# Kernel tuning notes

Hardware: AMD Instinct MI355X
Metric: run time of the kernel (lower is better)

The kernel has to match this reference:

```python
import jax, jax.numpy as jnp
import numpy as np

B, L, N = 4, 4096, 4096
COARSE_W, FINE_W = 1.0, 1000.0
PX_THRESH = 10.0


def setup_inputs() -> dict:
    key = jax.random.key(0)
    k1, k2, k3, k4, k5, k6 = jax.random.split(key, 6)
    # confidence matrix in (0,1] so log is finite
    cm_matrix = jax.random.uniform(k1, (B, L, L), jnp.float32, 1e-4, 1.0)
    # ground-truth match matrix: identity permutation (each i matches j=i)
    gt_matrix = jnp.tile(jnp.eye(L, dtype=jnp.float32)[None], (B, 1, 1))
    samples0 = jax.random.uniform(k2, (B, L, 2), jnp.float32, 0.0, 1000.0)
    samples1 = jax.random.uniform(k3, (B, L, 2), jnp.float32, 0.0, 1000.0)
    b_idx = jax.random.randint(k4, (N,), 0, B)
    i_idx = jax.random.randint(k5, (N,), 0, L)
    # predicted mkpts0 copied exactly from gt coords -> exact float equality match
    mkpts0 = jnp.concatenate([b_idx[:, None].astype(jnp.float32),
                              samples0[b_idx, i_idx]], axis=1)  # [N,3] = (b,x,y)
    noise = jax.random.normal(k6, (N, 2), jnp.float32) * 6.0  # some pass <10px gate, some not
    mkpts1 = samples1[b_idx, i_idx] + noise  # [N,2]
    return {"cm_matrix": cm_matrix, "gt_matrix": gt_matrix,
            "samples0": samples0, "samples1": samples1,
            "mkpts0": mkpts0, "mkpts1": mkpts1}


def _losses(cm_matrix, gt_matrix, samples0, samples1, mkpts0, mkpts1):
    b, l0, l1 = gt_matrix.shape
    # --- coarse CE loss ---
    coarse = (-gt_matrix * jnp.log(cm_matrix + 1e-6)).sum() / b

    # --- fine loss (vectorized first-match semantics) ---
    gt_mask = gt_matrix > 0                       # [B,L0,L1]
    gt_mask_v = gt_mask.any(axis=2)               # [B,L0] valid gt rows
    j_ids = jnp.argmax(gt_mask, axis=2)           # [B,L0] first True along j
    bb = jnp.broadcast_to(jnp.arange(b, dtype=samples0.dtype)[:, None], (b, l0))
    gt0 = jnp.concatenate([bb[..., None], samples0], axis=-1).reshape(b * l0, 3)  # (b,x,y)
    gt1 = jnp.take_along_axis(samples1, j_ids[:, :, None], axis=1).reshape(b * l0, 2)
    valid = gt_mask_v.reshape(-1)                 # [M]

    # eq[n,m]: predicted mkpts0[n] exactly equals gt row m (and row is valid)
    eq = (mkpts0[:, None, :] == gt0[None, :, :]).all(-1) & valid[None, :]  # [N,M]
    found = eq.any(axis=1)                        # [N]
    first = jnp.argmax(eq, axis=1)                # first matching gt row
    matched_gt1 = gt1[first]                      # [N,2]
    per_norm = jnp.linalg.norm(matched_gt1 - mkpts1, axis=1)  # [N]
    sel = found & (per_norm < PX_THRESH)
    cnt = sel.sum()
    fine = jnp.where(cnt > 0,
                     jnp.sum(per_norm * sel) / jnp.maximum(cnt, 1).astype(per_norm.dtype),
                     jnp.asarray(10.0, per_norm.dtype))
    fine = jnp.where(valid.any(), fine, jnp.asarray(1e-6, per_norm.dtype))
    # original does torch.tensor(loss, requires_grad=True): detaches from inputs
    fine = jax.lax.stop_gradient(fine)

    losses = COARSE_W * coarse + FINE_W * fine
    return jnp.stack([losses, coarse, fine])


def reference(cm_matrix, gt_matrix, samples0, samples1, mkpts0, mkpts1):
    # returns [losses, coarse_loss, fine_loss]
    return _losses(cm_matrix, gt_matrix, samples0, samples1, mkpts0, mkpts1)
```

## Files before the change

kernel.cpp:

```cpp
#include <hip/hip_runtime.h>
#include <climits>
#include <cstdint>


typedef float    f32x4 __attribute__((ext_vector_type(4)));
typedef unsigned u32x4 __attribute__((ext_vector_type(4)));

static constexpr int CGRID = 2048;
static constexpr int DEPTH = 8;

template <int LSHIFT>
__device__ __forceinline__ void coarse_proc4(
    float& local, const float* __restrict__ cm, int* __restrict__ jv,
    const f32x4 g, const unsigned v)
{
    const u32x4 u = __builtin_bit_cast(u32x4, g);
    if ((u.x | u.y | u.z | u.w) != 0u) {
        constexpr unsigned LMASK = (1u << LSHIFT) - 1u;
        const unsigned e   = v << 2;
        const unsigned row = e >> LSHIFT;
        const unsigned col = e & LMASK;
        #pragma unroll
        for (int k = 0; k < 4; ++k) {
            const float gk = g[k];
            if (gk != 0.0f) {
                local += gk * logf(__builtin_nontemporal_load(&cm[e + k]) + 1e-6f);
                if (gk > 0.0f) atomicMin(&jv[row], (int)(col + (unsigned)k));
            }
        }
    }
}

__device__ __forceinline__ void coarse_proc4_gen(
    float& local, const float* __restrict__ cm, int* __restrict__ jv,
    const f32x4 g, const unsigned v, const unsigned L)
{
    const u32x4 u = __builtin_bit_cast(u32x4, g);
    if ((u.x | u.y | u.z | u.w) != 0u) {
        const unsigned e   = v << 2;
        const unsigned row = e / L;
        const unsigned col = e - row * L;
        #pragma unroll
        for (int k = 0; k < 4; ++k) {
            const float gk = g[k];
            if (gk != 0.0f) {
                local += gk * logf(__builtin_nontemporal_load(&cm[e + k]) + 1e-6f);
                if (gk > 0.0f) atomicMin(&jv[row], (int)(col + (unsigned)k));
            }
        }
    }
}

template <int LSHIFT>
__global__ __launch_bounds__(256) void mc_coarse_flat(
    const float* __restrict__ cm, const float* __restrict__ gt,
    unsigned nvec, int* __restrict__ jv, float* __restrict__ partial)
{
    const unsigned stride = gridDim.x * blockDim.x;
    unsigned v = blockIdx.x * blockDim.x + threadIdx.x;
    const f32x4* __restrict__ g4 = reinterpret_cast<const f32x4*>(gt);

    float local = 0.0f;

    for (; v + (DEPTH - 1u) * stride < nvec; v += (unsigned)DEPTH * stride) {
        f32x4 g[DEPTH];
        #pragma unroll
        for (int m = 0; m < DEPTH; ++m)
            g[m] = __builtin_nontemporal_load(&g4[v + (unsigned)m * stride]);
        #pragma unroll
        for (int m = 0; m < DEPTH; ++m)
            coarse_proc4<LSHIFT>(local, cm, jv, g[m], v + (unsigned)m * stride);
    }
    for (; v < nvec; v += stride) {
        const f32x4 g = __builtin_nontemporal_load(&g4[v]);
        coarse_proc4<LSHIFT>(local, cm, jv, g, v);
    }

    #pragma unroll
    for (int o = 32; o; o >>= 1) local += __shfl_down(local, o);
    __shared__ float sc[4];
    if ((threadIdx.x & 63) == 0) sc[threadIdx.x >> 6] = local;
    __syncthreads();
    if (threadIdx.x == 0) partial[blockIdx.x] = sc[0] + sc[1] + sc[2] + sc[3];
}

__global__ __launch_bounds__(256) void mc_coarse_flat_gen(
    const float* __restrict__ cm, const float* __restrict__ gt,
    unsigned nvec, unsigned L, int* __restrict__ jv, float* __restrict__ partial)
{
    const unsigned stride = gridDim.x * blockDim.x;
    unsigned v = blockIdx.x * blockDim.x + threadIdx.x;
    const f32x4* __restrict__ g4 = reinterpret_cast<const f32x4*>(gt);

    float local = 0.0f;
    for (; v + (DEPTH - 1u) * stride < nvec; v += (unsigned)DEPTH * stride) {
        f32x4 g[DEPTH];
        #pragma unroll
        for (int m = 0; m < DEPTH; ++m)
            g[m] = __builtin_nontemporal_load(&g4[v + (unsigned)m * stride]);
        #pragma unroll
        for (int m = 0; m < DEPTH; ++m)
            coarse_proc4_gen(local, cm, jv, g[m], v + (unsigned)m * stride, L);
    }
    for (; v < nvec; v += stride) {
        const f32x4 g = __builtin_nontemporal_load(&g4[v]);
        coarse_proc4_gen(local, cm, jv, g, v, L);
    }

    #pragma unroll
    for (int o = 32; o; o >>= 1) local += __shfl_down(local, o);
    __shared__ float sc[4];
    if ((threadIdx.x & 63) == 0) sc[threadIdx.x >> 6] = local;
    __syncthreads();
    if (threadIdx.x == 0) partial[blockIdx.x] = sc[0] + sc[1] + sc[2] + sc[3];
}

__global__ __launch_bounds__(256) void mc_fine_kernel(
    const float* __restrict__ s0, const float* __restrict__ s1,
    const float* __restrict__ mk0, const float* __restrict__ mk1,
    const int* __restrict__ jv, int B, int L,
    float* __restrict__ pnbuf)
{
    const int n = blockIdx.x;
    const float bf = mk0[3 * n + 0];
    const float x  = mk0[3 * n + 1];
    const float y  = mk0[3 * n + 2];
    const int b = (int)bf;

    int best = INT_MAX;
    if ((float)b == bf && b >= 0 && b < B) {
        const float2* __restrict__ srow = reinterpret_cast<const float2*>(s0 + (size_t)b * L * 2);
        const int*    __restrict__ jrow = jv + (size_t)b * L;
        #pragma unroll 4
        for (int i = threadIdx.x; i < L; i += 256) {
            const float2 s = srow[i];
            if (s.x == x && s.y == y && jrow[i] < L) best = min(best, i);
        }
    }
    #pragma unroll
    for (int o = 32; o; o >>= 1) best = min(best, __shfl_down(best, o));

    __shared__ int sb[4];
    if ((threadIdx.x & 63) == 0) sb[threadIdx.x >> 6] = best;
    __syncthreads();

    if (threadIdx.x == 0) {
        best = min(min(sb[0], sb[1]), min(sb[2], sb[3]));
        float res = -1.0f;
        if (best != INT_MAX) {
            const int j = jv[(size_t)b * L + best];
            const float gx = s1[((size_t)b * L + j) * 2 + 0];
            const float gy = s1[((size_t)b * L + j) * 2 + 1];
            const float dx = gx - mk1[2 * n + 0];
            const float dy = gy - mk1[2 * n + 1];
            const float pn = sqrtf(dx * dx + dy * dy);
            if (pn < 10.0f) res = pn;
        }
        pnbuf[n] = res;
    }
}

__global__ __launch_bounds__(1024) void mc_finalize_kernel(
    const float* __restrict__ partial, int P,
    const int* __restrict__ jv, int M,
    const float* __restrict__ pnbuf, int N,
    float binv, int L, float* __restrict__ out)
{
    float csum = 0.0f, fsum = 0.0f;
    int vcnt = 0, fcnt = 0;
    for (int i = threadIdx.x; i < P; i += 1024) csum += partial[i];
    for (int i = threadIdx.x; i < M; i += 1024) vcnt += (jv[i] < L) ? 1 : 0;
    for (int i = threadIdx.x; i < N; i += 1024) {
        const float p = pnbuf[i];
        if (p >= 0.0f) { fsum += p; ++fcnt; }
    }
    #pragma unroll
    for (int o = 32; o; o >>= 1) {
        csum += __shfl_down(csum, o);
        vcnt += __shfl_down(vcnt, o);
        fsum += __shfl_down(fsum, o);
        fcnt += __shfl_down(fcnt, o);
    }
    __shared__ float sc[16], sf[16];
    __shared__ int   sv[16], sn[16];
    const int wid = threadIdx.x >> 6, lane = threadIdx.x & 63;
    if (lane == 0) { sc[wid] = csum; sv[wid] = vcnt; sf[wid] = fsum; sn[wid] = fcnt; }
    __syncthreads();
    if (threadIdx.x == 0) {
        float C = 0.0f, F = 0.0f; int V = 0, K = 0;
        const int nw = blockDim.x >> 6;
        for (int w = 0; w < nw; ++w) { C += sc[w]; V += sv[w]; F += sf[w]; K += sn[w]; }
        const float coarse = -C * binv;
        const float fine = (V > 0) ? ((K > 0) ? F / (float)K : 10.0f) : 1e-6f;
        out[0] = coarse + 1000.0f * fine;
        out[1] = coarse;
        out[2] = fine;
    }
}

extern "C" void kernel_launch(void* const* d_in, const int* in_sizes, int n_in,
                              void* d_out, int out_size, void* d_ws, size_t ws_size,
                              hipStream_t stream) {
    const float* cm  = (const float*)d_in[0];
    const float* gt  = (const float*)d_in[1];
    const float* s0  = (const float*)d_in[2];
    const float* s1  = (const float*)d_in[3];
    const float* mk0 = (const float*)d_in[4];
    const float* mk1 = (const float*)d_in[5];
    float* out = (float*)d_out;

    const int L = 2 * (in_sizes[0] / in_sizes[2]);
    const int B = in_sizes[2] / (2 * L);
    const int N = in_sizes[4] / 3;
    const int M = B * L;
    const unsigned nvec = (unsigned)(in_sizes[0] >> 2);

    int*   jv      = (int*)d_ws;
    float* pnbuf   = (float*)((char*)d_ws + (size_t)M * 4);
    float* partial = (float*)((char*)d_ws + (size_t)M * 4 + (size_t)N * 4);

    hipMemsetAsync(jv, 0x7F, (size_t)M * 4, stream);

    if (L == 4096) {
        mc_coarse_flat<12><<<CGRID, 256, 0, stream>>>(cm, gt, nvec, jv, partial);
    } else {
        mc_coarse_flat_gen<<<CGRID, 256, 0, stream>>>(cm, gt, nvec, (unsigned)L, jv, partial);
    }
    mc_fine_kernel<<<N, 256, 0, stream>>>(s0, s1, mk0, mk1, jv, B, L, pnbuf);
    mc_finalize_kernel<<<1, 1024, 0, stream>>>(partial, CGRID, jv, M, pnbuf, N,
                                               1.0f / (float)B, L, out);
}
```

Measured before the change: 468.9 us.

## Split coarse pass into sparse nonzero compaction scan and hit-processing kernel

The coarse pass becomes two kernels. The first streams the gt matrix and appends each nonzero (index, value) into a compacted list through a global atomic counter. The second kernel evaluates the log and atomicMin only for those entries, so the scan loop no longer carries log or cm-load work inline. The scan also switches from nontemporal loads to plain loads. Costs are a global atomic per nonzero, an extra launch and memset, and a spill path with float atomicAdd when the list capacity runs out.

Result: slower. 585.3 us (+24.8%).

```diff
diff --git a/kernel.cpp b/kernel.cpp
--- a/kernel.cpp
+++ b/kernel.cpp
@@ -6,107 +6,97 @@
 typedef float    f32x4 __attribute__((ext_vector_type(4)));
 typedef unsigned u32x4 __attribute__((ext_vector_type(4)));
 
-static constexpr int CGRID = 2048;
-static constexpr int DEPTH = 8;
-
-template <int LSHIFT>
-__device__ __forceinline__ void coarse_proc4(
-    float& local, const float* __restrict__ cm, int* __restrict__ jv,
-    const f32x4 g, const unsigned v)
-{
-    const u32x4 u = __builtin_bit_cast(u32x4, g);
-    if ((u.x | u.y | u.z | u.w) != 0u) {
-        constexpr unsigned LMASK = (1u << LSHIFT) - 1u;
-        const unsigned e   = v << 2;
-        const unsigned row = e >> LSHIFT;
-        const unsigned col = e & LMASK;
-        #pragma unroll
-        for (int k = 0; k < 4; ++k) {
-            const float gk = g[k];
-            if (gk != 0.0f) {
-                local += gk * logf(__builtin_nontemporal_load(&cm[e + k]) + 1e-6f);
-                if (gk > 0.0f) atomicMin(&jv[row], (int)(col + (unsigned)k));
-            }
-        }
-    }
-}
-
-__device__ __forceinline__ void coarse_proc4_gen(
-    float& local, const float* __restrict__ cm, int* __restrict__ jv,
-    const f32x4 g, const unsigned v, const unsigned L)
-{
-    const u32x4 u = __builtin_bit_cast(u32x4, g);
-    if ((u.x | u.y | u.z | u.w) != 0u) {
-        const unsigned e   = v << 2;
-        const unsigned row = e / L;
-        const unsigned col = e - row * L;
-        #pragma unroll
-        for (int k = 0; k < 4; ++k) {
-            const float gk = g[k];
-            if (gk != 0.0f) {
-                local += gk * logf(__builtin_nontemporal_load(&cm[e + k]) + 1e-6f);
-                if (gk > 0.0f) atomicMin(&jv[row], (int)(col + (unsigned)k));
-            }
-        }
-    }
-}
-
-template <int LSHIFT>
-__global__ __launch_bounds__(256) void mc_coarse_flat(
-    const float* __restrict__ cm, const float* __restrict__ gt,
-    unsigned nvec, int* __restrict__ jv, float* __restrict__ partial)
+static constexpr int      AGRID   = 2048;
+static constexpr int      DEPTH   = 8;
+static constexpr int      BGRID   = 256;
+static constexpr unsigned CAP_MAX = 4u << 20;
+
+struct Ent { unsigned idx; float val; };
+
+__global__ __launch_bounds__(256) void mc_scan(
+    const float* __restrict__ gt, unsigned nvec, unsigned L,
+    unsigned* __restrict__ gcnt, Ent* __restrict__ ents, unsigned cap,
+    const float* __restrict__ cm, int* __restrict__ jv,
+    float* __restrict__ spill)
 {
     const unsigned stride = gridDim.x * blockDim.x;
     unsigned v = blockIdx.x * blockDim.x + threadIdx.x;
     const f32x4* __restrict__ g4 = reinterpret_cast<const f32x4*>(gt);
-
-    float local = 0.0f;
 
     for (; v + (DEPTH - 1u) * stride < nvec; v += (unsigned)DEPTH * stride) {
         f32x4 g[DEPTH];
         #pragma unroll
         for (int m = 0; m < DEPTH; ++m)
-            g[m] = __builtin_nontemporal_load(&g4[v + (unsigned)m * stride]);
+            g[m] = g4[v + (unsigned)m * stride];
         #pragma unroll
-        for (int m = 0; m < DEPTH; ++m)
-            coarse_proc4<LSHIFT>(local, cm, jv, g[m], v + (unsigned)m * stride);
+        for (int m = 0; m < DEPTH; ++m) {
+            const u32x4 u = __builtin_bit_cast(u32x4, g[m]);
+            if ((u.x | u.y | u.z | u.w) != 0u) {
+                const unsigned e = (v + (unsigned)m * stride) << 2;
+                #pragma unroll
+                for (int k = 0; k < 4; ++k) {
+                    const float gk = g[m][k];
+                    if (gk != 0.0f) {
+                        const unsigned idx = atomicAdd(gcnt, 1u);
+                        if (idx < cap) {
+                            ents[idx].idx = e + (unsigned)k;
+                            ents[idx].val = gk;
+                        } else {
+                            atomicAdd(spill, gk * logf(cm[e + k] + 1e-6f));
+                            if (gk > 0.0f) {
+                                const unsigned ee = e + (unsigned)k;
+                                const unsigned row = ee / L;
+                                atomicMin(&jv[row], (int)(ee - row * L));
+                            }
+                        }
+                    }
+                }
+            }
+        }
     }
     for (; v < nvec; v += stride) {
-        const f32x4 g = __builtin_nontemporal_load(&g4[v]);
-        coarse_proc4<LSHIFT>(local, cm, jv, g, v);
-    }
-
-    #pragma unroll
-    for (int o = 32; o; o >>= 1) local += __shfl_down(local, o);
-    __shared__ float sc[4];
-    if ((threadIdx.x & 63) == 0) sc[threadIdx.x >> 6] = local;
-    __syncthreads();
-    if (threadIdx.x == 0) partial[blockIdx.x] = sc[0] + sc[1] + sc[2] + sc[3];
-}
-
-__global__ __launch_bounds__(256) void mc_coarse_flat_gen(
-    const float* __restrict__ cm, const float* __restrict__ gt,
-    unsigned nvec, unsigned L, int* __restrict__ jv, float* __restrict__ partial)
-{
-    const unsigned stride = gridDim.x * blockDim.x;
-    unsigned v = blockIdx.x * blockDim.x + threadIdx.x;
-    const f32x4* __restrict__ g4 = reinterpret_cast<const f32x4*>(gt);
-
+        const f32x4 g = g4[v];
+        const u32x4 u = __builtin_bit_cast(u32x4, g);
+        if ((u.x | u.y | u.z | u.w) != 0u) {
+            const unsigned e = v << 2;
+            #pragma unroll
+            for (int k = 0; k < 4; ++k) {
+                const float gk = g[k];
+                if (gk != 0.0f) {
+                    const unsigned idx = atomicAdd(gcnt, 1u);
+                    if (idx < cap) {
+                        ents[idx].idx = e + (unsigned)k;
+                        ents[idx].val = gk;
+                    } else {
+                        atomicAdd(spill, gk * logf(cm[e + k] + 1e-6f));
+                        if (gk > 0.0f) {
+                            const unsigned ee = e + (unsigned)k;
+                            const unsigned row = ee / L;
+                            atomicMin(&jv[row], (int)(ee - row * L));
+                        }
+                    }
+                }
+            }
+        }
+    }
+}
+
+__global__ __launch_bounds__(256) void mc_hits(
+    const Ent* __restrict__ ents, const unsigned* __restrict__ gcnt,
+    unsigned cap, const float* __restrict__ cm, unsigned L,
+    int* __restrict__ jv, float* __restrict__ partial)
+{
+    const unsigned n = min(*gcnt, cap);
     float local = 0.0f;
-    for (; v + (DEPTH - 1u) * stride < nvec; v += (unsigned)DEPTH * stride) {
-        f32x4 g[DEPTH];
-        #pragma unroll
-        for (int m = 0; m < DEPTH; ++m)
-            g[m] = __builtin_nontemporal_load(&g4[v + (unsigned)m * stride]);
-        #pragma unroll
-        for (int m = 0; m < DEPTH; ++m)
-            coarse_proc4_gen(local, cm, jv, g[m], v + (unsigned)m * stride, L);
-    }
-    for (; v < nvec; v += stride) {
-        const f32x4 g = __builtin_nontemporal_load(&g4[v]);
-        coarse_proc4_gen(local, cm, jv, g, v, L);
-    }
-
+    for (unsigned i = blockIdx.x * blockDim.x + threadIdx.x; i < n;
+         i += gridDim.x * blockDim.x) {
+        const Ent t = ents[i];
+        local += t.val * logf(cm[t.idx] + 1e-6f);
+        if (t.val > 0.0f) {
+            const unsigned row = t.idx / L;
+            atomicMin(&jv[row], (int)(t.idx - row * L));
+        }
+    }
     #pragma unroll
     for (int o = 32; o; o >>= 1) local += __shfl_down(local, o);
     __shared__ float sc[4];
@@ -162,6 +152,7 @@
 
 __global__ __launch_bounds__(1024) void mc_finalize_kernel(
     const float* __restrict__ partial, int P,
+    const float* __restrict__ spill,
     const int* __restrict__ jv, int M,
     const float* __restrict__ pnbuf, int N,
     float binv, int L, float* __restrict__ out)
@@ -187,7 +178,7 @@
     if (lane == 0) { sc[wid] = csum; sv[wid] = vcnt; sf[wid] = fsum; sn[wid] = fcnt; }
     __syncthreads();
     if (threadIdx.x == 0) {
-        float C = 0.0f, F = 0.0f; int V = 0, K = 0;
+        float C = *spill, F = 0.0f; int V = 0, K = 0;
         const int nw = blockDim.x >> 6;
         for (int w = 0; w < nw; ++w) { C += sc[w]; V += sv[w]; F += sf[w]; K += sn[w]; }
         const float coarse = -C * binv;
@@ -215,18 +206,26 @@
     const int M = B * L;
     const unsigned nvec = (unsigned)(in_sizes[0] >> 2);
 
-    int*   jv      = (int*)d_ws;
-    float* pnbuf   = (float*)((char*)d_ws + (size_t)M * 4);
-    float* partial = (float*)((char*)d_ws + (size_t)M * 4 + (size_t)N * 4);
-
+    char* p = (char*)d_ws;
+    unsigned* gcnt  = (unsigned*)p;
+    float*    spill = (float*)(p + 4);
+    int*      jv    = (int*)(p + 64);
+    float*    pnbuf = (float*)(p + 64 + (size_t)M * 4);
+    float*    partB = (float*)(p + 64 + (size_t)M * 4 + (size_t)N * 4);
+    size_t ents_off = 64 + (size_t)M * 4 + (size_t)N * 4 + (size_t)BGRID * 4;
+    ents_off = (ents_off + 63) & ~(size_t)63;
+    Ent* ents = (Ent*)(p + ents_off);
+    unsigned cap = 0;
+    if (ws_size > ents_off + 8)
+        cap = (unsigned)min((size_t)CAP_MAX, (ws_size - ents_off) / 8);
+
+    hipMemsetAsync(gcnt, 0, 8, stream);
     hipMemsetAsync(jv, 0x7F, (size_t)M * 4, stream);
 
-    if (L == 4096) {
-        mc_coarse_flat<12><<<CGRID, 256, 0, stream>>>(cm, gt, nvec, jv, partial);
-    } else {
-        mc_coarse_flat_gen<<<CGRID, 256, 0, stream>>>(cm, gt, nvec, (unsigned)L, jv, partial);
-    }
+    mc_scan<<<AGRID, 256, 0, stream>>>(gt, nvec, (unsigned)L, gcnt, ents, cap,
+                                       cm, jv, spill);
+    mc_hits<<<BGRID, 256, 0, stream>>>(ents, gcnt, cap, cm, (unsigned)L, jv, partB);
     mc_fine_kernel<<<N, 256, 0, stream>>>(s0, s1, mk0, mk1, jv, B, L, pnbuf);
-    mc_finalize_kernel<<<1, 1024, 0, stream>>>(partial, CGRID, jv, M, pnbuf, N,
+    mc_finalize_kernel<<<1, 1024, 0, stream>>>(partB, BGRID, spill, jv, M, pnbuf, N,
                                                1.0f / (float)B, L, out);
 }
```

## Compact sparse gt nonzeros into shared-memory queue before processing

Applied to the files above, without the earlier changes.

Instead of each thread doing the dependent cm load, log and atomicMin inline whenever it finds a nonzero in its gt vector, threads push nonzero (index, value) pairs into a per-block shared-memory queue. After a barrier, the whole block drains the queue with full lane utilization. The intent is to remove the divergent, latency-bound scattered loads from the streaming gt loop so the main loop stays bandwidth-bound. It adds shared atomics and a barrier, and falls back to inline processing once the queue overflows. It also drops the unrolled path in the generic kernel.

Result: no change. 472.2 us (+0.7%).

```diff
diff --git a/kernel.cpp b/kernel.cpp
--- a/kernel.cpp
+++ b/kernel.cpp
@@ -8,54 +8,20 @@
 
 static constexpr int CGRID = 2048;
 static constexpr int DEPTH = 8;
-
-template <int LSHIFT>
-__device__ __forceinline__ void coarse_proc4(
-    float& local, const float* __restrict__ cm, int* __restrict__ jv,
-    const f32x4 g, const unsigned v)
-{
-    const u32x4 u = __builtin_bit_cast(u32x4, g);
-    if ((u.x | u.y | u.z | u.w) != 0u) {
-        constexpr unsigned LMASK = (1u << LSHIFT) - 1u;
-        const unsigned e   = v << 2;
-        const unsigned row = e >> LSHIFT;
-        const unsigned col = e & LMASK;
-        #pragma unroll
-        for (int k = 0; k < 4; ++k) {
-            const float gk = g[k];
-            if (gk != 0.0f) {
-                local += gk * logf(__builtin_nontemporal_load(&cm[e + k]) + 1e-6f);
-                if (gk > 0.0f) atomicMin(&jv[row], (int)(col + (unsigned)k));
-            }
-        }
-    }
-}
-
-__device__ __forceinline__ void coarse_proc4_gen(
-    float& local, const float* __restrict__ cm, int* __restrict__ jv,
-    const f32x4 g, const unsigned v, const unsigned L)
-{
-    const u32x4 u = __builtin_bit_cast(u32x4, g);
-    if ((u.x | u.y | u.z | u.w) != 0u) {
-        const unsigned e   = v << 2;
-        const unsigned row = e / L;
-        const unsigned col = e - row * L;
-        #pragma unroll
-        for (int k = 0; k < 4; ++k) {
-            const float gk = g[k];
-            if (gk != 0.0f) {
-                local += gk * logf(__builtin_nontemporal_load(&cm[e + k]) + 1e-6f);
-                if (gk > 0.0f) atomicMin(&jv[row], (int)(col + (unsigned)k));
-            }
-        }
-    }
-}
+static constexpr int QCAP  = 1024;
 
 template <int LSHIFT>
 __global__ __launch_bounds__(256) void mc_coarse_flat(
     const float* __restrict__ cm, const float* __restrict__ gt,
     unsigned nvec, int* __restrict__ jv, float* __restrict__ partial)
 {
+    constexpr unsigned LMASK = (1u << LSHIFT) - 1u;
+    __shared__ unsigned qn;
+    __shared__ unsigned qidx[QCAP];
+    __shared__ float    qval[QCAP];
+    if (threadIdx.x == 0) qn = 0;
+    __syncthreads();
+
     const unsigned stride = gridDim.x * blockDim.x;
     unsigned v = blockIdx.x * blockDim.x + threadIdx.x;
     const f32x4* __restrict__ g4 = reinterpret_cast<const f32x4*>(gt);
@@ -68,12 +34,60 @@
         for (int m = 0; m < DEPTH; ++m)
             g[m] = __builtin_nontemporal_load(&g4[v + (unsigned)m * stride]);
         #pragma unroll
-        for (int m = 0; m < DEPTH; ++m)
-            coarse_proc4<LSHIFT>(local, cm, jv, g[m], v + (unsigned)m * stride);
+        for (int m = 0; m < DEPTH; ++m) {
+            const u32x4 u = __builtin_bit_cast(u32x4, g[m]);
+            if ((u.x | u.y | u.z | u.w) != 0u) {
+                const unsigned e = (v + (unsigned)m * stride) << 2;
+                #pragma unroll
+                for (int k = 0; k < 4; ++k) {
+                    const float gk = g[m][k];
+                    if (gk != 0.0f) {
+                        const unsigned qi = atomicAdd(&qn, 1u);
+                        if (qi < (unsigned)QCAP) {
+                            qidx[qi] = e + (unsigned)k;
+                            qval[qi] = gk;
+                        } else {
+                            local += gk * logf(cm[e + k] + 1e-6f);
+                            if (gk > 0.0f)
+                                atomicMin(&jv[(e + k) >> LSHIFT],
+                                          (int)((e + k) & LMASK));
+                        }
+                    }
+                }
+            }
+        }
     }
     for (; v < nvec; v += stride) {
         const f32x4 g = __builtin_nontemporal_load(&g4[v]);
-        coarse_proc4<LSHIFT>(local, cm, jv, g, v);
+        const u32x4 u = __builtin_bit_cast(u32x4, g);
+        if ((u.x | u.y | u.z | u.w) != 0u) {
+            const unsigned e = v << 2;
+            #pragma unroll
+            for (int k = 0; k < 4; ++k) {
+                const float gk = g[k];
+                if (gk != 0.0f) {
+                    const unsigned qi = atomicAdd(&qn, 1u);
+                    if (qi < (unsigned)QCAP) {
+                        qidx[qi] = e + (unsigned)k;
+                        qval[qi] = gk;
+                    } else {
+                        local += gk * logf(cm[e + k] + 1e-6f);
+                        if (gk > 0.0f)
+                            atomicMin(&jv[(e + k) >> LSHIFT],
+                                      (int)((e + k) & LMASK));
+                    }
+                }
+            }
+        }
+    }
+
+    __syncthreads();
+    const unsigned n = min(qn, (unsigned)QCAP);
+    for (unsigned i = threadIdx.x; i < n; i += 256) {
+        const unsigned idx = qidx[i];
+        const float    gv  = qval[i];
+        local += gv * logf(cm[idx] + 1e-6f);
+        if (gv > 0.0f) atomicMin(&jv[idx >> LSHIFT], (int)(idx & LMASK));
     }
 
     #pragma unroll
@@ -88,23 +102,49 @@
     const float* __restrict__ cm, const float* __restrict__ gt,
     unsigned nvec, unsigned L, int* __restrict__ jv, float* __restrict__ partial)
 {
+    __shared__ unsigned qn;
+    __shared__ unsigned qidx[QCAP];
+    __shared__ float    qval[QCAP];
+    if (threadIdx.x == 0) qn = 0;
+    __syncthreads();
+
     const unsigned stride = gridDim.x * blockDim.x;
     unsigned v = blockIdx.x * blockDim.x + threadIdx.x;
     const f32x4* __restrict__ g4 = reinterpret_cast<const f32x4*>(gt);
 
     float local = 0.0f;
-    for (; v + (DEPTH - 1u) * stride < nvec; v += (unsigned)DEPTH * stride) {
-        f32x4 g[DEPTH];
-        #pragma unroll
-        for (int m = 0; m < DEPTH; ++m)
-            g[m] = __builtin_nontemporal_load(&g4[v + (unsigned)m * stride]);
-        #pragma unroll
-        for (int m = 0; m < DEPTH; ++m)
-            coarse_proc4_gen(local, cm, jv, g[m], v + (unsigned)m * stride, L);
-    }
     for (; v < nvec; v += stride) {
         const f32x4 g = __builtin_nontemporal_load(&g4[v]);
-        coarse_proc4_gen(local, cm, jv, g, v, L);
+        const u32x4 u = __builtin_bit_cast(u32x4, g);
+        if ((u.x | u.y | u.z | u.w) != 0u) {
+            const unsigned e = v << 2;
+            #pragma unroll
+            for (int k = 0; k < 4; ++k) {
+                const float gk = g[k];
+                if (gk != 0.0f) {
+                    const unsigned qi = atomicAdd(&qn, 1u);
+                    if (qi < (unsigned)QCAP) {
+                        qidx[qi] = e + (unsigned)k;
+                        qval[qi] = gk;
+                    } else {
+                        const unsigned ee = e + (unsigned)k;
+                        const unsigned row = ee / L;
+                        local += gk * logf(cm[ee] + 1e-6f);
+                        if (gk > 0.0f) atomicMin(&jv[row], (int)(ee - row * L));
+                    }
+                }
+            }
+        }
+    }
+
+    __syncthreads();
+    const unsigned n = min(qn, (unsigned)QCAP);
+    for (unsigned i = threadIdx.x; i < n; i += 256) {
+        const unsigned idx = qidx[i];
+        const float    gv  = qval[i];
+        const unsigned row = idx / L;
+        local += gv * logf(cm[idx] + 1e-6f);
+        if (gv > 0.0f) atomicMin(&jv[row], (int)(idx - row * L));
     }
 
     #pragma unroll
```
